# Optimization experiments

Hardware: AMD Instinct MI355X
Metric: run time of the kernel (lower is better)

## Reference

```python
import jax, jax.numpy as jnp
import numpy as np

NUM_LEVELS = 12
LEVEL_DIM = 2
BASE_RES = 16
DESIRED_RES = 8192
LOG2_HASH = 21
PRIMES = (1, 2654435761, 805459861)


def _level_specs(D):
    # torch-ngp GridEncoder table layout: per-level (offset, size, scale, res, use_hash)
    f = (DESIRED_RES / BASE_RES) ** (1.0 / (NUM_LEVELS - 1))
    specs = []
    offset = 0
    for l in range(NUM_LEVELS):
        scale = BASE_RES * (f ** l) - 1.0
        res = int(np.ceil(scale)) + 1
        dense = (res + 1) ** D  # align_corners=False -> stride uses res+1
        params = min(2 ** LOG2_HASH, dense)
        params = int(np.ceil(params / 8) * 8)
        specs.append((offset, params, scale, res, dense > 2 ** LOG2_HASH))
        offset += params
    return specs, offset


def grid_encode(x, table, D):
    # x: [N, D] in [-1, 1]; table: [T, LEVEL_DIM]. Returns [N, NUM_LEVELS*LEVEL_DIM].
    x01 = (x + 1.0) * 0.5  # (inputs + bound) / (2*bound), bound=1
    specs, _ = _level_specs(D)
    feats = []
    for (off, hsize, scale, res, use_hash) in specs:
        pos = x01 * scale + 0.5  # align_corners=False
        pg_f = jnp.floor(pos)
        frac = pos - pg_f          # [N, D]
        pg = pg_f.astype(jnp.uint32)
        acc = jnp.zeros((x.shape[0], LEVEL_DIM), dtype=table.dtype)
        for c in range(2 ** D):  # 4 or 8 corners, static unroll
            w = None
            idx = jnp.zeros((x.shape[0],), dtype=jnp.uint32)
            stride = 1
            for d in range(D):
                bit = (c >> d) & 1
                coord = pg[:, d] + jnp.uint32(bit)
                wd = frac[:, d] if bit else (1.0 - frac[:, d])
                w = wd if w is None else w * wd
                if use_hash:
                    idx = idx ^ (coord * jnp.uint32(PRIMES[d]))  # uint32 wraparound xor-hash
                else:
                    idx = idx + coord * jnp.uint32(stride)
                    stride *= (res + 1)
            gidx = (idx % jnp.uint32(hsize)).astype(jnp.int32) + off
            acc = acc + w[:, None] * table[gidx]
        feats.append(acc)
    return jnp.concatenate(feats, axis=-1)


def mlp(feat, w1, b1, w2, b2):
    h = jax.nn.relu(feat @ w1 + b1)
    return h @ w2 + b2


def setup_inputs() -> dict:
    key = jax.random.key(0)
    ks = jax.random.split(key, 16)
    B, P = 4096, 1000
    line = jax.random.uniform(ks[0], (B, 2), dtype=jnp.float32)
    line_points = jax.random.uniform(ks[1], (B, P, 3), dtype=jnp.float32)
    gt_o = jax.random.uniform(ks[2], (B, P), dtype=jnp.float32)
    _, tot2 = _level_specs(2)
    _, tot3 = _level_specs(3)
    table_conf = jax.random.uniform(ks[3], (tot2, LEVEL_DIM), jnp.float32, -1e-4, 1e-4)
    table_op = jax.random.uniform(ks[4], (tot3, LEVEL_DIM), jnp.float32, -1e-4, 1e-4)
    F = NUM_LEVELS * LEVEL_DIM  # 24
    w1_c = jax.random.normal(ks[5], (F, 64), jnp.float32) * 0.1
    b1_c = jnp.zeros((64,), jnp.float32)
    w2_c = jax.random.normal(ks[6], (64, 1), jnp.float32) * 0.1
    b2_c = jnp.zeros((1,), jnp.float32)
    w1_o = jax.random.normal(ks[7], (F, 64), jnp.float32) * 0.1
    b1_o = jnp.zeros((64,), jnp.float32)
    w2_o = jax.random.normal(ks[8], (64, 1), jnp.float32) * 0.1
    b2_o = jnp.zeros((1,), jnp.float32)
    return {"line": line, "line_points": line_points, "gt_o": gt_o,
            "table_conf": table_conf, "w1_c": w1_c, "b1_c": b1_c, "w2_c": w2_c, "b2_c": b2_c,
            "table_op": table_op, "w1_o": w1_o, "b1_o": b1_o, "w2_o": w2_o, "b2_o": b2_o}


def reference(line, line_points, gt_o, table_conf, w1_c, b1_c, w2_c, b2_c,
              table_op, w1_o, b1_o, w2_o, b2_o):
    B, P, _ = line_points.shape
    pts = line_points.reshape(B * P, 3)
    feat_o = grid_encode(pts, table_op, 3)             # [B*P, 24]
    opacity = mlp(feat_o, w1_o, b1_o, w2_o, b2_o).reshape(B, P)  # squeeze(2)
    feat_c = grid_encode(line, table_conf, 2)          # [B, 24]
    confidence = mlp(feat_c, w1_c, b1_c, w2_c, b2_c)[:, 0]       # squeeze(1)
    loss1 = jnp.abs(opacity - gt_o)
    col_w = jnp.where(jnp.arange(P) < 500, 4.0 / 3.0, 2.0 / 3.0).astype(loss1.dtype)
    loss1 = loss1 * col_w[None, :]
    loss = jnp.exp(-confidence) * loss1.mean(axis=1) + confidence
    return loss.mean()
```

## Files before the change

### kernel.cpp

```cpp
#include <hip/hip_runtime.h>
#include <hip/hip_bf16.h>
#include <math.h>

#define NLEV 12
#define B_LINES 4096
#define P_PTS 1000
#define FP8_SCALE 65536.0f
#define FP8_ISCALE (1.0f / 65536.0f)
#define NBLK_PER_LEV 256

typedef unsigned short ushort_t;
typedef __attribute__((ext_vector_type(8))) short short8_t;
typedef __attribute__((ext_vector_type(4))) float f32x4;

struct LevelSpec {
    unsigned off;
    unsigned mask;
    float    scale;
    unsigned R;
};
struct Specs { LevelSpec L[NLEV]; };
struct HashScales { float s[8]; };

static unsigned compute_specs(int D, Specs* sp) {
    double f = pow(8192.0 / 16.0, 1.0 / 11.0);
    unsigned offset = 0;
    for (int l = 0; l < NLEV; ++l) {
        double scale = 16.0 * pow(f, (double)l) - 1.0;
        int res = (int)ceil(scale) + 1;
        unsigned long long dense = 1ull;
        for (int d = 0; d < D; ++d) dense *= (unsigned long long)(res + 1);
        unsigned long long params = dense > (1ull << 21) ? (1ull << 21) : dense;
        params = ((params + 7ull) / 8ull) * 8ull;
        sp->L[l].off   = offset;
        sp->L[l].mask  = (unsigned)params - 1u;
        sp->L[l].scale = (float)scale;
        sp->L[l].R     = (unsigned)(res + 1);
        offset += (unsigned)params;
    }
    return offset;
}


__device__ __forceinline__ float block_reduce_256(float v) {
    __shared__ float red[256];
    int tid = threadIdx.x;
    red[tid] = v;
    __syncthreads();
    #pragma unroll
    for (int s = 128; s >= 1; s >>= 1) {
        if (tid < s) red[tid] += red[tid + s];
        __syncthreads();
    }
    return red[0];
}

__device__ __forceinline__ unsigned short f32_to_bf16_bits(float f) {
    unsigned u = __float_as_uint(f);
    unsigned r = (u + 0x7fffu + ((u >> 16) & 1u)) >> 16;
    return (unsigned short)r;
}

__device__ __forceinline__ void store_nt_feat(__hip_bfloat162* p,
                                              float a0, float a1) {
    union { __hip_bfloat162 b; unsigned u; } cv;
    cv.b.x = __float2bfloat16(a0 * FP8_ISCALE);
    cv.b.y = __float2bfloat16(a1 * FP8_ISCALE);
    __builtin_nontemporal_store(cv.u, (unsigned*)p);
}

__device__ __forceinline__ int pair_entry(const ushort_t* __restrict__ base,
                                          unsigned H) {
    unsigned w = *(const unsigned*)(base + (H & ~1u));
    return (int)((w >> ((H & 1u) << 4)) & 0xffffu);
}

__device__ __forceinline__ float mlp_24_64_1(const float feat[24],
        const float* __restrict__ w1, const float* __restrict__ b1,
        const float* __restrict__ w2, const float* __restrict__ b2) {
    float o = b2[0];
    #pragma unroll
    for (int half = 0; half < 2; ++half) {
        float h[32];
        #pragma unroll
        for (int j = 0; j < 32; ++j) h[j] = b1[half * 32 + j];
        #pragma unroll
        for (int k = 0; k < 24; ++k) {
            float fv = feat[k];
            #pragma unroll
            for (int j = 0; j < 32; ++j)
                h[j] = fmaf(fv, w1[k * 64 + half * 32 + j], h[j]);
        }
        #pragma unroll
        for (int j = 0; j < 32; ++j)
            o = fmaf(fmaxf(h[j], 0.f), w2[half * 32 + j], o);
    }
    return o;
}

__global__ void __launch_bounds__(256) convert_kernel(
        const float2* __restrict__ in, ushort_t* __restrict__ out, int n) {
    int i = blockIdx.x * 256 + threadIdx.x;
    if (i >= n) return;
    float2 v;
    v.x = __builtin_nontemporal_load(&in[i].x);
    v.y = __builtin_nontemporal_load(&in[i].y);
    int p = __builtin_amdgcn_cvt_pk_fp8_f32(v.x * FP8_SCALE, v.y * FP8_SCALE,
                                            0, false);
    __builtin_nontemporal_store((ushort_t)(p & 0xffff), &out[i]);
}

__global__ void __launch_bounds__(256) enc_dense_kernel(
        const float* __restrict__ pts, int pbase, int npts,
        const ushort_t* __restrict__ tabq,
        __hip_bfloat162* __restrict__ feats,
        Specs sp) {
    int i = blockIdx.x * 256 + threadIdx.x;
    if (i >= npts) return;
    int gp = pbase + i;
    float x0 = (pts[3 * gp + 0] + 1.f) * 0.5f;
    float x1 = (pts[3 * gp + 1] + 1.f) * 0.5f;
    float x2 = (pts[3 * gp + 2] + 1.f) * 0.5f;
    #pragma unroll
    for (int l = 0; l < 4; ++l) {
        const LevelSpec L = sp.L[l];
        float p0 = x0 * L.scale + 0.5f;
        float p1 = x1 * L.scale + 0.5f;
        float p2 = x2 * L.scale + 0.5f;
        float f0 = floorf(p0), f1 = floorf(p1), f2 = floorf(p2);
        float r0 = p0 - f0, r1 = p1 - f1, r2 = p2 - f2;
        float u0 = 1.f - r0, u1 = 1.f - r1, u2 = 1.f - r2;
        unsigned g0 = (unsigned)f0, g1 = (unsigned)f1, g2 = (unsigned)f2;
        const ushort_t* __restrict__ base = tabq + L.off;
        unsigned R = L.R, R2 = R * R;
        unsigned y0 = g1 * R, y1 = y0 + R;
        unsigned z0 = g2 * R2, z1 = z0 + R2;
        int t[8];
        #pragma unroll
        for (int cz = 0; cz < 4; ++cz) {
            unsigned idx0 = g0 + ((cz & 1) ? y1 : y0) + ((cz & 2) ? z1 : z0);
            t[2 * cz]     = pair_entry(base, idx0);
            t[2 * cz + 1] = pair_entry(base, idx0 + 1u);
        }
        float a0 = 0.f, a1 = 0.f;
        #pragma unroll
        for (int c = 0; c < 8; ++c) {
            float w = ((c & 1) ? r0 : u0) * ((c & 2) ? r1 : u1)
                    * ((c & 4) ? r2 : u2);
            a0 = fmaf(w, __builtin_amdgcn_cvt_f32_fp8(t[c], 0), a0);
            a1 = fmaf(w, __builtin_amdgcn_cvt_f32_fp8(t[c], 1), a1);
        }
        store_nt_feat(&feats[(size_t)l * npts + i], a0, a1);
    }
}

struct HashPt { unsigned h[8]; float r0, r1, r2; };

__device__ __forceinline__ HashPt hash_addrs(
        const float* __restrict__ pts, int gp, float scale, unsigned m) {
    float x0 = (pts[3 * gp + 0] + 1.f) * 0.5f;
    float x1 = (pts[3 * gp + 1] + 1.f) * 0.5f;
    float x2 = (pts[3 * gp + 2] + 1.f) * 0.5f;
    float p0 = x0 * scale + 0.5f;
    float p1 = x1 * scale + 0.5f;
    float p2 = x2 * scale + 0.5f;
    float f0 = floorf(p0), f1 = floorf(p1), f2 = floorf(p2);
    HashPt o;
    o.r0 = p0 - f0; o.r1 = p1 - f1; o.r2 = p2 - f2;
    unsigned g0 = (unsigned)f0, g1 = (unsigned)f1, g2 = (unsigned)f2;
    unsigned y0 = g1 * 2654435761u, y1 = y0 + 2654435761u;
    unsigned z0 = g2 * 805459861u,  z1 = z0 + 805459861u;
    #pragma unroll
    for (int c = 0; c < 8; ++c) {
        unsigned h = (g0 + ((c & 1) ? 1u : 0u))
                   ^ ((c & 2) ? y1 : y0) ^ ((c & 4) ? z1 : z0);
        o.h[c] = h & m;
    }
    return o;
}

__device__ __forceinline__ void interp_store(
        const int t[8], const HashPt& hp, __hip_bfloat162* dst) {
    float u0 = 1.f - hp.r0, u1 = 1.f - hp.r1, u2 = 1.f - hp.r2;
    float a0 = 0.f, a1 = 0.f;
    #pragma unroll
    for (int c = 0; c < 8; ++c) {
        float w = ((c & 1) ? hp.r0 : u0) * ((c & 2) ? hp.r1 : u1)
                * ((c & 4) ? hp.r2 : u2);
        a0 = fmaf(w, __builtin_amdgcn_cvt_f32_fp8(t[c], 0), a0);
        a1 = fmaf(w, __builtin_amdgcn_cvt_f32_fp8(t[c], 1), a1);
    }
    store_nt_feat(dst, a0, a1);
}

__global__ void __launch_bounds__(256) enc_hash_all_kernel(
        const float* __restrict__ pts, int pbase, int npts,
        const ushort_t* __restrict__ tabq, unsigned hash_off0,
        HashScales hs,
        __hip_bfloat162* __restrict__ feats) {
    const int lev = blockIdx.x & 7;
    const int bpl = blockIdx.x >> 3;
    const int tid = threadIdx.x;
    float scale = hs.s[0];
    #pragma unroll
    for (int k = 1; k < 8; ++k) if (lev == k) scale = hs.s[k];
    const ushort_t* __restrict__ base =
        tabq + hash_off0 + ((unsigned)lev << 21);
    const unsigned m = (1u << 21) - 1u;
    __hip_bfloat162* __restrict__ slab = feats + (size_t)(4 + lev) * npts;

    const int stride = NBLK_PER_LEV * 1024;
    for (int p0 = bpl * 1024; p0 < npts; p0 += stride) {
        int  idx[4];
        bool val[4];
        HashPt hp[4];
        int  t[4][8];
        #pragma unroll
        for (int q = 0; q < 4; ++q) {
            int i = p0 + q * 256 + tid;
            val[q] = i < npts;
            idx[q] = val[q] ? i : npts - 1;
            hp[q]  = hash_addrs(pts, pbase + idx[q], scale, m);
            #pragma unroll
            for (int c = 0; c < 8; ++c)
                t[q][c] = pair_entry(base, hp[q].h[c]);
        }
        #pragma unroll
        for (int q = 0; q < 4; ++q)
            if (val[q]) interp_store(t[q], hp[q], slab + idx[q]);
    }
}

__global__ void __launch_bounds__(256) mlp_loss_mfma_kernel(
        const unsigned* __restrict__ feats, int npts,
        const float* __restrict__ gt, int line0,
        const float* __restrict__ w1, const float* __restrict__ b1,
        const float* __restrict__ w2, const float* __restrict__ b2,
        float* __restrict__ S) {
    const int line_local = blockIdx.x;
    const int tid  = threadIdx.x;
    const int wave = tid >> 6;
    const int lane = tid & 63;
    const int c = lane & 15;
    const int g = lane >> 4;

    short8_t bfrag[4];
    #pragma unroll
    for (int nb = 0; nb < 4; ++nb) {
        #pragma unroll
        for (int i = 0; i < 8; ++i) {
            int k = g * 8 + i;
            float v = (k < 24) ? w1[k * 64 + nb * 16 + c] : 0.f;
            bfrag[nb][i] = (short)f32_to_bf16_bits(v);
        }
    }
    float b1v[4], w2v[4];
    #pragma unroll
    for (int nb = 0; nb < 4; ++nb) {
        b1v[nb] = b1[nb * 16 + c];
        w2v[nb] = w2[nb * 16 + c];
    }
    const float b2v = b2[0];

    const size_t lbase = (size_t)line_local * P_PTS;
    float lsum = 0.f;

    for (int it = 0; it < 16; ++it) {
        const int base16 = it * 64 + wave * 16;
        int prow = base16 + c;
        int pcl  = prow < P_PTS ? prow : P_PTS - 1;
        size_t pidx = lbase + (size_t)pcl;
        union { unsigned u[4]; short8_t v; } a;
        if (g < 3) {
            #pragma unroll
            for (int s = 0; s < 4; ++s)
                a.u[s] = feats[(size_t)(g * 4 + s) * npts + pidx];
        } else {
            a.u[0] = 0u; a.u[1] = 0u; a.u[2] = 0u; a.u[3] = 0u;
        }
        f32x4 acc[4];
        #pragma unroll
        for (int nb = 0; nb < 4; ++nb) {
            f32x4 ci = {b1v[nb], b1v[nb], b1v[nb], b1v[nb]};
            acc[nb] = __builtin_amdgcn_mfma_f32_16x16x32_bf16(
                a.v, bfrag[nb], ci, 0, 0, 0);
        }
        float part[4];
        #pragma unroll
        for (int r = 0; r < 4; ++r) {
            float s = fmaxf(acc[0][r], 0.f) * w2v[0];
            s = fmaf(fmaxf(acc[1][r], 0.f), w2v[1], s);
            s = fmaf(fmaxf(acc[2][r], 0.f), w2v[2], s);
            s = fmaf(fmaxf(acc[3][r], 0.f), w2v[3], s);
            part[r] = s;
        }
        #pragma unroll
        for (int off = 1; off < 16; off <<= 1) {
            #pragma unroll
            for (int r = 0; r < 4; ++r)
                part[r] += __shfl_xor(part[r], off);
        }
        if (c < 4) {
            int p = base16 + g * 4 + c;
            if (p < P_PTS) {
                float op = part[c] + b2v;
                float gv = gt[(size_t)(line0 + line_local) * P_PTS + p];
                float cw = (p < 500) ? (float)(4.0 / 3.0) : (float)(2.0 / 3.0);
                lsum += fabsf(op - gv) * cw;
            }
        }
    }
    float tot = block_reduce_256(lsum);
    if (tid == 0) S[line0 + line_local] = tot;
}

__global__ void __launch_bounds__(256) opacity_mono_kernel(
        const float* __restrict__ pts, const float* __restrict__ gt,
        const float2* __restrict__ tab,
        const float* __restrict__ w1, const float* __restrict__ b1,
        const float* __restrict__ w2, const float* __restrict__ b2,
        float* __restrict__ S, Specs sp) {
    const int b = blockIdx.x;
    const int tid = threadIdx.x;
    float lsum = 0.f;
    for (int p = tid; p < P_PTS; p += 256) {
        const int i = b * P_PTS + p;
        float x0 = (pts[3 * i + 0] + 1.f) * 0.5f;
        float x1 = (pts[3 * i + 1] + 1.f) * 0.5f;
        float x2 = (pts[3 * i + 2] + 1.f) * 0.5f;
        float feat[24];
        #pragma unroll
        for (int l = 0; l < NLEV; ++l) {
            const LevelSpec L = sp.L[l];
            float p0 = x0 * L.scale + 0.5f;
            float p1 = x1 * L.scale + 0.5f;
            float p2 = x2 * L.scale + 0.5f;
            float f0 = floorf(p0), f1 = floorf(p1), f2 = floorf(p2);
            float r0 = p0 - f0, r1 = p1 - f1, r2 = p2 - f2;
            float u0 = 1.f - r0, u1 = 1.f - r1, u2 = 1.f - r2;
            unsigned g0 = (unsigned)f0, g1 = (unsigned)f1, g2 = (unsigned)f2;
            float a0 = 0.f, a1 = 0.f;
            if (l >= 4) {
                unsigned y0 = g1 * 2654435761u, y1 = y0 + 2654435761u;
                unsigned z0 = g2 * 805459861u,  z1 = z0 + 805459861u;
                unsigned m = L.mask;
                #pragma unroll
                for (int c = 0; c < 8; ++c) {
                    unsigned h = (g0 + ((c & 1) ? 1u : 0u))
                               ^ ((c & 2) ? y1 : y0) ^ ((c & 4) ? z1 : z0);
                    float2 t = tab[L.off + (h & m)];
                    float w = ((c & 1) ? r0 : u0) * ((c & 2) ? r1 : u1)
                            * ((c & 4) ? r2 : u2);
                    a0 = fmaf(w, t.x, a0); a1 = fmaf(w, t.y, a1);
                }
            } else {
                unsigned R = L.R, R2 = R * R;
                unsigned y0 = g1 * R, y1 = y0 + R;
                unsigned z0 = g2 * R2, z1 = z0 + R2;
                #pragma unroll
                for (int c = 0; c < 8; ++c) {
                    unsigned idx = (g0 + ((c & 1) ? 1u : 0u))
                                 + ((c & 2) ? y1 : y0) + ((c & 4) ? z1 : z0);
                    float2 t = tab[L.off + idx];
                    float w = ((c & 1) ? r0 : u0) * ((c & 2) ? r1 : u1)
                            * ((c & 4) ? r2 : u2);
                    a0 = fmaf(w, t.x, a0); a1 = fmaf(w, t.y, a1);
                }
            }
            feat[2 * l] = a0; feat[2 * l + 1] = a1;
        }
        float op = mlp_24_64_1(feat, w1, b1, w2, b2);
        float cw = (p < 500) ? (float)(4.0 / 3.0) : (float)(2.0 / 3.0);
        lsum += fabsf(op - gt[i]) * cw;
    }
    float tot = block_reduce_256(lsum);
    if (tid == 0) S[b] = tot;
}

__global__ void __launch_bounds__(256) conf_kernel(
        const float* __restrict__ line, const float2* __restrict__ tab,
        const float* __restrict__ w1, const float* __restrict__ b1,
        const float* __restrict__ w2, const float* __restrict__ b2,
        const float* __restrict__ S, float* __restrict__ partial, Specs sp) {
    const int b = blockIdx.x * 256 + threadIdx.x;
    float x0 = (line[2 * b + 0] + 1.f) * 0.5f;
    float x1 = (line[2 * b + 1] + 1.f) * 0.5f;
    float feat[24];
    #pragma unroll
    for (int l = 0; l < NLEV; ++l) {
        const unsigned off = sp.L[l].off;
        const float scale = sp.L[l].scale;
        float p0 = x0 * scale + 0.5f;
        float p1 = x1 * scale + 0.5f;
        float f0 = floorf(p0), f1 = floorf(p1);
        float r0 = p0 - f0, r1 = p1 - f1;
        float u0 = 1.f - r0, u1 = 1.f - r1;
        unsigned g0 = (unsigned)f0, g1 = (unsigned)f1;
        unsigned idx0, idx1, idx2, idx3;
        if (l >= 8) {
            const unsigned mask = sp.L[l].mask;
            unsigned a1 = g1 * 2654435761u, bb1 = a1 + 2654435761u;
            idx0 = (g0 ^ a1) & mask;
            idx1 = ((g0 + 1u) ^ a1) & mask;
            idx2 = (g0 ^ bb1) & mask;
            idx3 = ((g0 + 1u) ^ bb1) & mask;
        } else {
            const unsigned R = sp.L[l].R;
            unsigned a1 = g1 * R, bb1 = a1 + R;
            idx0 = g0 + a1; idx1 = g0 + 1u + a1;
            idx2 = g0 + bb1; idx3 = g0 + 1u + bb1;
        }
        float2 t0 = tab[off + idx0], t1 = tab[off + idx1];
        float2 t2 = tab[off + idx2], t3 = tab[off + idx3];
        float w0 = u0 * u1, w1c = r0 * u1, w2c = u0 * r1, w3 = r0 * r1;
        feat[2 * l]     = w0 * t0.x + w1c * t1.x + w2c * t2.x + w3 * t3.x;
        feat[2 * l + 1] = w0 * t0.y + w1c * t1.y + w2c * t2.y + w3 * t3.y;
    }
    float conf = mlp_24_64_1(feat, w1, b1, w2, b2);
    float term = expf(-conf) * (S[b] * (1.0f / (float)P_PTS)) + conf;
    float tot = block_reduce_256(term);
    if (threadIdx.x == 0) partial[blockIdx.x] = tot;
}

__global__ void final_kernel(const float* __restrict__ partial,
                             float* __restrict__ out) {
    if (threadIdx.x == 0) {
        float s = 0.f;
        for (int i = 0; i < 16; ++i) s += partial[i];
        out[0] = s * (1.0f / (float)B_LINES);
    }
}


extern "C" void kernel_launch(void* const* d_in, const int* in_sizes, int n_in,
                              void* d_out, int out_size, void* d_ws, size_t ws_size,
                              hipStream_t stream) {
    const float* line    = (const float*)d_in[0];
    const float* pts     = (const float*)d_in[1];
    const float* gt      = (const float*)d_in[2];
    const float* table_c = (const float*)d_in[3];
    const float* w1_c    = (const float*)d_in[4];
    const float* b1_c    = (const float*)d_in[5];
    const float* w2_c    = (const float*)d_in[6];
    const float* b2_c    = (const float*)d_in[7];
    const float* table_o = (const float*)d_in[8];
    const float* w1_o    = (const float*)d_in[9];
    const float* b1_o    = (const float*)d_in[10];
    const float* w2_o    = (const float*)d_in[11];
    const float* b2_o    = (const float*)d_in[12];
    (void)in_sizes; (void)n_in; (void)out_size;

    Specs sp3, sp2;
    unsigned tot3 = compute_specs(3, &sp3);
    compute_specs(2, &sp2);

    size_t tabB = (((size_t)tot3 * 2) + 255) & ~(size_t)255;
    size_t head = tabB + (size_t)B_LINES * 4 + 64;
    head = (head + 63) & ~(size_t)63;
    long max_lines = 0;
    if (ws_size > head + 64)
        max_lines = (long)((ws_size - head - 64) / ((size_t)P_PTS * 12 * 4));

    float* S       = (float*)((char*)d_ws + tabB);
    float* partial = S + B_LINES;

    if (max_lines >= 64) {
        ushort_t* tabq = (ushort_t*)d_ws;
        __hip_bfloat162* featbuf = (__hip_bfloat162*)((char*)d_ws + head);

        int chunk_lines = (int)(max_lines < B_LINES ? max_lines : B_LINES);
        int nch = (B_LINES + chunk_lines - 1) / chunk_lines;

        HashScales hs;
        for (int k = 0; k < 8; ++k) hs.s[k] = sp3.L[4 + k].scale;
        const unsigned hash_off0 = sp3.L[4].off;

        convert_kernel<<<((int)tot3 + 255) / 256, 256, 0, stream>>>(
            (const float2*)table_o, tabq, (int)tot3);

        for (int ch = 0; ch < nch; ++ch) {
            int line0 = ch * chunk_lines;
            int lines = B_LINES - line0 < chunk_lines ? B_LINES - line0
                                                      : chunk_lines;
            int npts = lines * P_PTS;
            int pbase = line0 * P_PTS;
            int nblk = (npts + 255) / 256;
            enc_dense_kernel<<<nblk, 256, 0, stream>>>(
                pts, pbase, npts, tabq, featbuf, sp3);
            enc_hash_all_kernel<<<NBLK_PER_LEV * 8, 256, 0, stream>>>(
                pts, pbase, npts, tabq, hash_off0, hs, featbuf);
            mlp_loss_mfma_kernel<<<lines, 256, 0, stream>>>(
                (const unsigned*)featbuf, npts, gt, line0,
                w1_o, b1_o, w2_o, b2_o, S);
        }
    } else {
        opacity_mono_kernel<<<B_LINES, 256, 0, stream>>>(
            pts, gt, (const float2*)table_o, w1_o, b1_o, w2_o, b2_o, S, sp3);
    }

    conf_kernel<<<16, 256, 0, stream>>>(
        line, (const float2*)table_c, w1_c, b1_c, w2_c, b2_c, S, partial, sp2);
    final_kernel<<<1, 64, 0, stream>>>(partial, (float*)d_out);
}
```

Baseline: 1.361 ms.

## Fuse dense-level encoding into MLP loss kernel via shared-memory features

Drops the separate dense-level encode kernel and computes the four dense levels per line inside the MLP/loss kernel, staging the packed bf16 features in LDS instead of writing and re-reading them from global memory. The hash feature buffer shrinks to 8 levels, so more lines fit in each workspace chunk, and the gt and hash-feature loads become nontemporal. The cost is 16KB of LDS per block, which may lower occupancy, and a serial encode phase ahead of the MFMA work in each block.

```diff
diff --git a/kernel.cpp b/kernel.cpp
--- a/kernel.cpp
+++ b/kernel.cpp
@@ -61,12 +61,15 @@
     return (unsigned short)r;
 }
 
-__device__ __forceinline__ void store_nt_feat(__hip_bfloat162* p,
-                                              float a0, float a1) {
+__device__ __forceinline__ unsigned pack_feat(float a0, float a1) {
     union { __hip_bfloat162 b; unsigned u; } cv;
     cv.b.x = __float2bfloat16(a0 * FP8_ISCALE);
     cv.b.y = __float2bfloat16(a1 * FP8_ISCALE);
-    __builtin_nontemporal_store(cv.u, (unsigned*)p);
+    return cv.u;
+}
+
+__device__ __forceinline__ void store_nt_u32(unsigned v, unsigned* p) {
+    __builtin_nontemporal_store(v, p);
 }
 
 __device__ __forceinline__ int pair_entry(const ushort_t* __restrict__ base,
@@ -108,50 +111,6 @@
     int p = __builtin_amdgcn_cvt_pk_fp8_f32(v.x * FP8_SCALE, v.y * FP8_SCALE,
                                             0, false);
     __builtin_nontemporal_store((ushort_t)(p & 0xffff), &out[i]);
-}
-
-__global__ void __launch_bounds__(256) enc_dense_kernel(
-        const float* __restrict__ pts, int pbase, int npts,
-        const ushort_t* __restrict__ tabq,
-        __hip_bfloat162* __restrict__ feats,
-        Specs sp) {
-    int i = blockIdx.x * 256 + threadIdx.x;
-    if (i >= npts) return;
-    int gp = pbase + i;
-    float x0 = (pts[3 * gp + 0] + 1.f) * 0.5f;
-    float x1 = (pts[3 * gp + 1] + 1.f) * 0.5f;
-    float x2 = (pts[3 * gp + 2] + 1.f) * 0.5f;
-    #pragma unroll
-    for (int l = 0; l < 4; ++l) {
-        const LevelSpec L = sp.L[l];
-        float p0 = x0 * L.scale + 0.5f;
-        float p1 = x1 * L.scale + 0.5f;
-        float p2 = x2 * L.scale + 0.5f;
-        float f0 = floorf(p0), f1 = floorf(p1), f2 = floorf(p2);
-        float r0 = p0 - f0, r1 = p1 - f1, r2 = p2 - f2;
-        float u0 = 1.f - r0, u1 = 1.f - r1, u2 = 1.f - r2;
-        unsigned g0 = (unsigned)f0, g1 = (unsigned)f1, g2 = (unsigned)f2;
-        const ushort_t* __restrict__ base = tabq + L.off;
-        unsigned R = L.R, R2 = R * R;
-        unsigned y0 = g1 * R, y1 = y0 + R;
-        unsigned z0 = g2 * R2, z1 = z0 + R2;
-        int t[8];
-        #pragma unroll
-        for (int cz = 0; cz < 4; ++cz) {
-            unsigned idx0 = g0 + ((cz & 1) ? y1 : y0) + ((cz & 2) ? z1 : z0);
-            t[2 * cz]     = pair_entry(base, idx0);
-            t[2 * cz + 1] = pair_entry(base, idx0 + 1u);
-        }
-        float a0 = 0.f, a1 = 0.f;
-        #pragma unroll
-        for (int c = 0; c < 8; ++c) {
-            float w = ((c & 1) ? r0 : u0) * ((c & 2) ? r1 : u1)
-                    * ((c & 4) ? r2 : u2);
-            a0 = fmaf(w, __builtin_amdgcn_cvt_f32_fp8(t[c], 0), a0);
-            a1 = fmaf(w, __builtin_amdgcn_cvt_f32_fp8(t[c], 1), a1);
-        }
-        store_nt_feat(&feats[(size_t)l * npts + i], a0, a1);
-    }
 }
 
 struct HashPt { unsigned h[8]; float r0, r1, r2; };
@@ -180,7 +139,7 @@
 }
 
 __device__ __forceinline__ void interp_store(
-        const int t[8], const HashPt& hp, __hip_bfloat162* dst) {
+        const int t[8], const HashPt& hp, unsigned* dst) {
     float u0 = 1.f - hp.r0, u1 = 1.f - hp.r1, u2 = 1.f - hp.r2;
     float a0 = 0.f, a1 = 0.f;
     #pragma unroll
@@ -190,14 +149,14 @@
         a0 = fmaf(w, __builtin_amdgcn_cvt_f32_fp8(t[c], 0), a0);
         a1 = fmaf(w, __builtin_amdgcn_cvt_f32_fp8(t[c], 1), a1);
     }
-    store_nt_feat(dst, a0, a1);
+    store_nt_u32(pack_feat(a0, a1), dst);
 }
 
 __global__ void __launch_bounds__(256) enc_hash_all_kernel(
         const float* __restrict__ pts, int pbase, int npts,
         const ushort_t* __restrict__ tabq, unsigned hash_off0,
         HashScales hs,
-        __hip_bfloat162* __restrict__ feats) {
+        unsigned* __restrict__ feats) {
     const int lev = blockIdx.x & 7;
     const int bpl = blockIdx.x >> 3;
     const int tid = threadIdx.x;
@@ -207,7 +166,7 @@
     const ushort_t* __restrict__ base =
         tabq + hash_off0 + ((unsigned)lev << 21);
     const unsigned m = (1u << 21) - 1u;
-    __hip_bfloat162* __restrict__ slab = feats + (size_t)(4 + lev) * npts;
+    unsigned* __restrict__ slab = feats + (size_t)lev * npts;
 
     const int stride = NBLK_PER_LEV * 1024;
     for (int p0 = bpl * 1024; p0 < npts; p0 += stride) {
@@ -231,14 +190,58 @@
     }
 }
 
-__global__ void __launch_bounds__(256) mlp_loss_mfma_kernel(
-        const unsigned* __restrict__ feats, int npts,
+__global__ void __launch_bounds__(256) mlp_loss_fused_kernel(
+        const float* __restrict__ pts,
+        const unsigned* __restrict__ hfeats, int npts,
         const float* __restrict__ gt, int line0,
+        const ushort_t* __restrict__ tabq,
         const float* __restrict__ w1, const float* __restrict__ b1,
         const float* __restrict__ w2, const float* __restrict__ b2,
-        float* __restrict__ S) {
+        float* __restrict__ S, Specs sp) {
+    __shared__ unsigned ldsd[4 * P_PTS];
     const int line_local = blockIdx.x;
+    const int line = line0 + line_local;
     const int tid  = threadIdx.x;
+
+    for (int p = tid; p < P_PTS; p += 256) {
+        int gp = line * P_PTS + p;
+        float x0 = (pts[3 * gp + 0] + 1.f) * 0.5f;
+        float x1 = (pts[3 * gp + 1] + 1.f) * 0.5f;
+        float x2 = (pts[3 * gp + 2] + 1.f) * 0.5f;
+        #pragma unroll
+        for (int l = 0; l < 4; ++l) {
+            const LevelSpec L = sp.L[l];
+            float p0 = x0 * L.scale + 0.5f;
+            float p1 = x1 * L.scale + 0.5f;
+            float p2 = x2 * L.scale + 0.5f;
+            float f0 = floorf(p0), f1 = floorf(p1), f2 = floorf(p2);
+            float r0 = p0 - f0, r1 = p1 - f1, r2 = p2 - f2;
+            float u0 = 1.f - r0, u1 = 1.f - r1, u2 = 1.f - r2;
+            unsigned g0 = (unsigned)f0, g1 = (unsigned)f1, g2 = (unsigned)f2;
+            const ushort_t* __restrict__ base = tabq + L.off;
+            unsigned R = L.R, R2 = R * R;
+            unsigned y0 = g1 * R, y1 = y0 + R;
+            unsigned z0 = g2 * R2, z1 = z0 + R2;
+            int t[8];
+            #pragma unroll
+            for (int cz = 0; cz < 4; ++cz) {
+                unsigned i0 = g0 + ((cz & 1) ? y1 : y0) + ((cz & 2) ? z1 : z0);
+                t[2 * cz]     = pair_entry(base, i0);
+                t[2 * cz + 1] = pair_entry(base, i0 + 1u);
+            }
+            float a0 = 0.f, a1 = 0.f;
+            #pragma unroll
+            for (int c = 0; c < 8; ++c) {
+                float w = ((c & 1) ? r0 : u0) * ((c & 2) ? r1 : u1)
+                        * ((c & 4) ? r2 : u2);
+                a0 = fmaf(w, __builtin_amdgcn_cvt_f32_fp8(t[c], 0), a0);
+                a1 = fmaf(w, __builtin_amdgcn_cvt_f32_fp8(t[c], 1), a1);
+            }
+            ldsd[l * P_PTS + p] = pack_feat(a0, a1);
+        }
+    }
+    __syncthreads();
+
     const int wave = tid >> 6;
     const int lane = tid & 63;
     const int c = lane & 15;
@@ -271,10 +274,15 @@
         int pcl  = prow < P_PTS ? prow : P_PTS - 1;
         size_t pidx = lbase + (size_t)pcl;
         union { unsigned u[4]; short8_t v; } a;
-        if (g < 3) {
+        if (g == 0) {
             #pragma unroll
             for (int s = 0; s < 4; ++s)
-                a.u[s] = feats[(size_t)(g * 4 + s) * npts + pidx];
+                a.u[s] = ldsd[s * P_PTS + pcl];
+        } else if (g < 3) {
+            #pragma unroll
+            for (int s = 0; s < 4; ++s)
+                a.u[s] = __builtin_nontemporal_load(
+                    &hfeats[(size_t)((g - 1) * 4 + s) * npts + pidx]);
         } else {
             a.u[0] = 0u; a.u[1] = 0u; a.u[2] = 0u; a.u[3] = 0u;
         }
@@ -304,14 +312,15 @@
             int p = base16 + g * 4 + c;
             if (p < P_PTS) {
                 float op = part[c] + b2v;
-                float gv = gt[(size_t)(line0 + line_local) * P_PTS + p];
+                float gv = __builtin_nontemporal_load(
+                    &gt[(size_t)line * P_PTS + p]);
                 float cw = (p < 500) ? (float)(4.0 / 3.0) : (float)(2.0 / 3.0);
                 lsum += fabsf(op - gv) * cw;
             }
         }
     }
     float tot = block_reduce_256(lsum);
-    if (tid == 0) S[line0 + line_local] = tot;
+    if (tid == 0) S[line] = tot;
 }
 
 __global__ void __launch_bounds__(256) opacity_mono_kernel(
@@ -459,14 +468,14 @@
     head = (head + 63) & ~(size_t)63;
     long max_lines = 0;
     if (ws_size > head + 64)
-        max_lines = (long)((ws_size - head - 64) / ((size_t)P_PTS * 12 * 4));
+        max_lines = (long)((ws_size - head - 64) / ((size_t)P_PTS * 8 * 4));
 
     float* S       = (float*)((char*)d_ws + tabB);
     float* partial = S + B_LINES;
 
     if (max_lines >= 64) {
         ushort_t* tabq = (ushort_t*)d_ws;
-        __hip_bfloat162* featbuf = (__hip_bfloat162*)((char*)d_ws + head);
+        unsigned* featbuf = (unsigned*)((char*)d_ws + head);
 
         int chunk_lines = (int)(max_lines < B_LINES ? max_lines : B_LINES);
         int nch = (B_LINES + chunk_lines - 1) / chunk_lines;
@@ -484,14 +493,11 @@
                                                       : chunk_lines;
             int npts = lines * P_PTS;
             int pbase = line0 * P_PTS;
-            int nblk = (npts + 255) / 256;
-            enc_dense_kernel<<<nblk, 256, 0, stream>>>(
-                pts, pbase, npts, tabq, featbuf, sp3);
             enc_hash_all_kernel<<<NBLK_PER_LEV * 8, 256, 0, stream>>>(
                 pts, pbase, npts, tabq, hash_off0, hs, featbuf);
-            mlp_loss_mfma_kernel<<<lines, 256, 0, stream>>>(
-                (const unsigned*)featbuf, npts, gt, line0,
-                w1_o, b1_o, w2_o, b2_o, S);
+            mlp_loss_fused_kernel<<<lines, 256, 0, stream>>>(
+                pts, featbuf, npts, gt, line0, tabq,
+                w1_o, b1_o, w2_o, b2_o, S, sp3);
         }
     } else {
         opacity_mono_kernel<<<B_LINES, 256, 0, stream>>>(
```

Result: slower. 1.458 ms (+7.1%).
